# Performance work log

Measured on AMD Instinct MI355X. Metric: run time of the kernel, lower is better.

Reference implementation:

```python
import jax, jax.numpy as jnp
import numpy as np
import math

NUM_HEADS = 16
HEAD_SIZE = 64
QKT_MEAN = 0.0
QKT_STD = 0.05
APPLY_NOISE = True
NOISE_KEY = jax.random.key(42)


def quantize_activation_8bit(x):
    max_abs = jnp.maximum(jnp.max(jnp.abs(x)), 1e-08)
    scale = max_abs / 127.0
    return jnp.clip(jnp.round(x / scale), -127, 127) * scale


def quantize_weight_4bit(w):
    max_abs = jnp.maximum(jnp.max(jnp.abs(w)), 1e-08)
    scale = max_abs / 7.0
    return jnp.clip(jnp.round(w / scale), -7, 7) * scale


def setup_inputs() -> dict:
    key = jax.random.key(0)
    k1, k2, k3, k4 = jax.random.split(key, 4)
    B, S, D = 4, 1024, 1024
    hidden_states = jax.random.normal(k1, (B, S, D), dtype=jnp.float32)
    attention_mask = jnp.zeros((B, 1, 1, S), dtype=jnp.float32)
    # nn.Linear weights are [out_features, in_features]
    w_scale = 1.0 / math.sqrt(D)
    Wq = jax.random.normal(k2, (D, D), dtype=jnp.float32) * w_scale
    Wk = jax.random.normal(k3, (D, D), dtype=jnp.float32) * w_scale
    Wv = jax.random.normal(k4, (D, D), dtype=jnp.float32) * w_scale
    return {"hidden_states": hidden_states, "attention_mask": attention_mask,
            "Wq": Wq, "Wk": Wk, "Wv": Wv}


def _split_heads(x):
    B, S, _ = x.shape
    return x.reshape(B, S, NUM_HEADS, HEAD_SIZE).transpose(0, 2, 1, 3)  # [B,H,S,Dh]


def reference(hidden_states, attention_mask, Wq, Wk, Wv):
    h_q = quantize_activation_8bit(hidden_states)
    h_k = quantize_activation_8bit(hidden_states)
    Q = _split_heads(jnp.einsum('bsd,od->bso', h_q, quantize_weight_4bit(Wq)))
    K = _split_heads(jnp.einsum('bsd,od->bso', h_k, quantize_weight_4bit(Wk)))
    V = _split_heads(jnp.einsum('bsd,od->bso', hidden_states, quantize_weight_4bit(Wv)))
    qkt = jnp.einsum('bhqd,bhkd->bhqk', Q, K) / math.sqrt(HEAD_SIZE)
    if APPLY_NOISE and QKT_STD > 0:
        noise = jax.random.normal(NOISE_KEY, qkt.shape, dtype=qkt.dtype) * QKT_STD + QKT_MEAN
        qkt = qkt + noise
    qkt = qkt + attention_mask  # [B,1,1,S] broadcasts over [B,H,S,S]
    attn_weights = jax.nn.softmax(qkt, axis=-1)  # dropout is identity in eval
    ctx = jnp.einsum('bhqk,bhkd->bhqd', attn_weights, V)
    B, H, S, Dh = ctx.shape
    ctx = ctx.transpose(0, 2, 1, 3).reshape(B, S, H * Dh)
    return ctx
```

## Files before the change

### kernel.cpp

```cpp
#include <hip/hip_runtime.h>
#include <hip/hip_bf16.h>

typedef unsigned short u16;
typedef unsigned int u32;
typedef __bf16 bf16x8 __attribute__((ext_vector_type(8)));
typedef float f32x4 __attribute__((ext_vector_type(4)));

#define MFMA16(a, b, c) __builtin_amdgcn_mfma_f32_16x16x32_bf16((a), (b), (c), 0, 0, 0)

static __device__ __forceinline__ float bfbits2f(u32 b) {
    union { u32 u; float f; } c; c.u = b << 16; return c.f;
}
static __device__ __forceinline__ u32 f2bfbits(float f) {
    union { float f; u32 u; } c; c.f = f;
    return (c.u + 0x7FFFu + ((c.u >> 16) & 1u)) >> 16;
}
static __device__ __forceinline__ u32 f2bfbits_exact(float f) {
    union { float f; u32 u; } c; c.f = f;
    return c.u >> 16;
}
static __device__ __forceinline__ u32 pack_bf16x2(float lo, float hi) {
    float2 v; v.x = lo; v.y = hi;
    union { __hip_bfloat162 h; u32 u; } c;
    c.h = __float22bfloat162_rn(v);
    return c.u;
}

static __device__ __forceinline__ void noise_pu8(const u32* __restrict__ idx,
                                                 float* __restrict__ pu) {
    const u32 K1 = 42u, K2 = 0x1BD11BF0u;
    u32 x0[8], x1[8];
#pragma unroll
    for (int d = 0; d < 8; d++) { x0[d] = 0u; x1[d] = idx[d] + K1; }
#define TFR(R)                                            \
    _Pragma("unroll") for (int d = 0; d < 8; d++) {       \
        x0[d] += x1[d];                                   \
        x1[d] = __builtin_rotateleft32(x1[d], R) ^ x0[d]; \
    }
#define INJ(A, B)                                         \
    _Pragma("unroll") for (int d = 0; d < 8; d++) {       \
        x0[d] += (A); x1[d] += (B);                       \
    }
    TFR(13) TFR(15) TFR(26) TFR(6)  INJ(K1, K2 + 1u)
    TFR(17) TFR(29) TFR(16) TFR(24) INJ(K2, 2u)
    TFR(13) TFR(15) TFR(26) TFR(6)  INJ(0u, K1 + 3u)
    TFR(17) TFR(29) TFR(16) TFR(24) INJ(K1, K2 + 4u)
    TFR(13) TFR(15) TFR(26) TFR(6)  INJ(K2, 5u)
#undef TFR
#undef INJ
#pragma unroll
    for (int d = 0; d < 8; d++) {
        u32 bits = x0[d] ^ x1[d];
        float v2 = __uint_as_float((bits >> 9) | 0x40000000u);
        float u = v2 - 3.0f;
        float t = fmaf(-u, u, 1.0f);
        float L2 = __log2f(t);
        L2 = fmaxf(L2, -7.2134752f);
        float z = fmaf(L2, -0.69314718f, -2.5f);
        float p = 2.81022636e-08f;
        p = fmaf(p, z, 3.43273939e-07f);
        p = fmaf(p, z, -3.5233877e-06f);
        p = fmaf(p, z, -4.39150654e-06f);
        p = fmaf(p, z, 0.00021858087f);
        p = fmaf(p, z, -0.00125372503f);
        p = fmaf(p, z, -0.00417768164f);
        p = fmaf(p, z, 0.246640727f);
        p = fmaf(p, z, 1.50140941f);
        pu[d] = p * u;
    }
}

__global__ __launch_bounds__(256) void absmax_k(const float* __restrict__ h,
                                                const float* __restrict__ wq,
                                                const float* __restrict__ wk,
                                                const float* __restrict__ wv,
                                                u32* __restrict__ slots) {
    int t = blockIdx.y;
    const float* src = (t == 0) ? h : (t == 1) ? wq : (t == 2) ? wk : wv;
    int n4 = ((t == 0) ? 4096 * 1024 : 1024 * 1024) / 4;
    u32 mx = 0;
    int tid = threadIdx.x;
    for (int i = blockIdx.x * blockDim.x + tid; i < n4; i += gridDim.x * blockDim.x) {
        uint4 v = ((const uint4*)src)[i];
        mx = max(mx, v.x & 0x7FFFFFFFu);
        mx = max(mx, v.y & 0x7FFFFFFFu);
        mx = max(mx, v.z & 0x7FFFFFFFu);
        mx = max(mx, v.w & 0x7FFFFFFFu);
    }
    __shared__ u32 red[256];
    red[tid] = mx;
    __syncthreads();
    for (int s = 128; s > 0; s >>= 1) {
        if (tid < s) red[tid] = max(red[tid], red[tid + s]);
        __syncthreads();
    }
    if (tid == 0) atomicMax(&slots[t], red[0]);
}

__global__ __launch_bounds__(256) void prequant_all(const float* __restrict__ hidden,
                                                    const float* __restrict__ wq,
                                                    const float* __restrict__ wk,
                                                    const float* __restrict__ wv,
                                                    u16* __restrict__ hq,
                                                    u16* __restrict__ hbf,
                                                    u16* __restrict__ wqi,
                                                    u16* __restrict__ wki,
                                                    u16* __restrict__ wvi,
                                                    const u32* __restrict__ slots) {
    int y = blockIdx.y;
    const float* src = (y == 0) ? hidden : (y == 1) ? wq : (y == 2) ? wk : wv;
    u16* dqi = (y == 0) ? hq : (y == 1) ? wqi : (y == 2) ? wki : wvi;
    u16* draw = (y == 0) ? hbf : nullptr;
    float qmax = (y == 0) ? 127.0f : 7.0f;
    int n8 = ((y == 0) ? 4096 * 1024 : 1024 * 1024) / 8;

    float amax = fmaxf(__uint_as_float(slots[y]), 1e-8f);
    float scale = amax / qmax;
    for (int i = blockIdx.x * blockDim.x + threadIdx.x; i < n8; i += gridDim.x * blockDim.x) {
        float4 a = ((const float4*)src)[2 * i];
        float4 b = ((const float4*)src)[2 * i + 1];
        float x[8] = {a.x, a.y, a.z, a.w, b.x, b.y, b.z, b.w};
        u16 qi[8], rw[8];
#pragma unroll
        for (int j = 0; j < 8; j++) {
            float q = fminf(fmaxf(rintf(x[j] / scale), -qmax), qmax);
            qi[j] = (u16)f2bfbits_exact(q);
            rw[j] = (u16)f2bfbits(x[j]);
        }
        *(uint4*)(dqi + 8 * (size_t)i) = *(const uint4*)qi;
        if (draw) *(uint4*)(draw + 8 * (size_t)i) = *(const uint4*)rw;
    }
}

__global__ __launch_bounds__(256, 2) void qkv_gemm_all(const u16* __restrict__ hq,
                                                       const u16* __restrict__ hbf,
                                                       const u16* __restrict__ wqi,
                                                       const u16* __restrict__ wki,
                                                       const u16* __restrict__ wvi,
                                                       const u32* __restrict__ slots,
                                                       u16* __restrict__ Qb,
                                                       u16* __restrict__ Kb,
                                                       u16* __restrict__ Vtb) {
    __shared__ __align__(16) u16 As[128 * 40];
    __shared__ __align__(16) u16 Bs[128 * 40];
    int z = blockIdx.z;
    const u16* A  = (z < 2) ? hq : hbf;
    const u16* Bw = (z == 0) ? wqi : (z == 1) ? wki : wvi;
    u16* outp     = (z == 0) ? Qb : (z == 1) ? Kb : Vtb;
    int transOut = (z == 2);
    float s_a = fmaxf(__uint_as_float(slots[0]), 1e-8f) / 127.0f;
    float s_w = fmaxf(__uint_as_float(slots[z + 1]), 1e-8f) / 7.0f;
    float oscale = (z < 2) ? (s_a * s_w) : s_w;

    int tid = threadIdx.x;
    int srow = tid >> 2, scol = (tid & 3) * 8;
    int mbase = blockIdx.x * 128, nbase = blockIdx.y * 128;
    int lane = tid & 63, w = tid >> 6;
    int wv_m = w & 1, wv_n = w >> 1;
    int quad = lane >> 4, l16 = lane & 15;

    f32x4 acc[4][4];
#pragma unroll
    for (int i = 0; i < 4; i++)
#pragma unroll
        for (int j = 0; j < 4; j++) acc[i][j] = (f32x4){0.f, 0.f, 0.f, 0.f};

    const u16* aptr0 = A + (size_t)(mbase + srow) * 1024 + scol;
    const u16* aptr1 = A + (size_t)(mbase + 64 + srow) * 1024 + scol;
    const u16* bptr0 = Bw + (size_t)(nbase + srow) * 1024 + scol;
    const u16* bptr1 = Bw + (size_t)(nbase + 64 + srow) * 1024 + scol;

    for (int k0 = 0; k0 < 1024; k0 += 32) {
        uint4 a0 = *(const uint4*)(aptr0 + k0);
        uint4 a1 = *(const uint4*)(aptr1 + k0);
        uint4 b0 = *(const uint4*)(bptr0 + k0);
        uint4 b1 = *(const uint4*)(bptr1 + k0);
        __syncthreads();
        *(uint4*)(As + srow * 40 + scol) = a0;
        *(uint4*)(As + (64 + srow) * 40 + scol) = a1;
        *(uint4*)(Bs + srow * 40 + scol) = b0;
        *(uint4*)(Bs + (64 + srow) * 40 + scol) = b1;
        __syncthreads();
        bf16x8 af[4], bfr[4];
#pragma unroll
        for (int mt = 0; mt < 4; mt++)
            af[mt] = *(const bf16x8*)(As + (wv_m * 64 + mt * 16 + l16) * 40 + quad * 8);
#pragma unroll
        for (int nt = 0; nt < 4; nt++)
            bfr[nt] = *(const bf16x8*)(Bs + (wv_n * 64 + nt * 16 + l16) * 40 + quad * 8);
#pragma unroll
        for (int mt = 0; mt < 4; mt++)
#pragma unroll
            for (int nt = 0; nt < 4; nt++)
                acc[mt][nt] = MFMA16(af[mt], bfr[nt], acc[mt][nt]);
    }

#pragma unroll
    for (int mt = 0; mt < 4; mt++)
#pragma unroll
        for (int nt = 0; nt < 4; nt++)
#pragma unroll
            for (int r = 0; r < 4; r++) {
                float val = acc[mt][nt][r] * oscale;
                int m = mbase + wv_m * 64 + mt * 16 + quad * 4 + r;
                int o = nbase + wv_n * 64 + nt * 16 + l16;
                int b = m >> 10, s = m & 1023;
                int hh = o >> 6, dh = o & 63;
                size_t off = transOut ? (((size_t)(b * 16 + hh) * 64 + dh) * 1024 + s)
                                      : (((size_t)(b * 16 + hh) * 1024 + s) * 64 + dh);
                outp[off] = (u16)f2bfbits(val);
            }
}

__global__ __launch_bounds__(256, 2) void attn_kernel(const u16* __restrict__ Q,
                                                      const u16* __restrict__ K,
                                                      const u16* __restrict__ Vt,
                                                      const float* __restrict__ mask,
                                                      float* __restrict__ O0,
                                                      float* __restrict__ O1,
                                                      float* __restrict__ l0,
                                                      float* __restrict__ l1) {
    __shared__ __align__(16) u16 Plds[2][4][16][40];
    int qt = blockIdx.x, h = blockIdx.y;
    int b = blockIdx.z & 3, split = blockIdx.z >> 2;
    int bh = b * 16 + h;
    int tid = threadIdx.x, wv = tid >> 6, lane = tid & 63;
    int quad = lane >> 4, l16 = lane & 15;
    int q0 = qt * 64 + wv * 16;
    int ks0 = split * 512;

    float* Obuf = split ? O1 : O0;
    float* lbuf = split ? l1 : l0;

    const u16* Qb = Q + (size_t)bh * 1024 * 64;
    const u16* Kb = K + (size_t)bh * 1024 * 64;
    const u16* Vb = Vt + (size_t)bh * 64 * 1024;

    bf16x8 aq0 = *(const bf16x8*)(Qb + (q0 + l16) * 64 + quad * 8);
    bf16x8 aq1 = *(const bf16x8*)(Qb + (q0 + l16) * 64 + 32 + quad * 8);

    f32x4 oacc[4];
#pragma unroll
    for (int i = 0; i < 4; i++) oacc[i] = (f32x4){0.f, 0.f, 0.f, 0.f};
    float lsum[4] = {0.f, 0.f, 0.f, 0.f};

    u16* Pw0 = &Plds[0][wv][0][0];
    u16* Pw1 = &Plds[1][wv][0][0];
    u32 idxbase = ((u32)bh * 1024u + (u32)(q0 + quad * 4)) * 1024u;
    const float* maskb = mask + b * 1024;

    for (int ks = ks0; ks < ks0 + 512; ks += 32) {
        f32x4 s0 = (f32x4){0.f, 0.f, 0.f, 0.f};
        f32x4 s1 = (f32x4){0.f, 0.f, 0.f, 0.f};
        const u16* Kt = Kb + (size_t)ks * 64;
        bf16x8 bk0 = *(const bf16x8*)(Kt + l16 * 64 + quad * 8);
        bf16x8 bk1 = *(const bf16x8*)(Kt + l16 * 64 + 32 + quad * 8);
        bf16x8 bk2 = *(const bf16x8*)(Kt + (16 + l16) * 64 + quad * 8);
        bf16x8 bk3 = *(const bf16x8*)(Kt + (16 + l16) * 64 + 32 + quad * 8);
        s0 = MFMA16(aq0, bk0, s0);
        s0 = MFMA16(aq1, bk1, s0);
        s1 = MFMA16(aq0, bk2, s1);
        s1 = MFMA16(aq1, bk3, s1);

        int kg0 = ks + l16;
        float mk0 = maskb[kg0];
        float mk1 = maskb[kg0 + 16];

        u32 idxs[8];
        float pu[8];
#pragma unroll
        for (int r = 0; r < 4; r++) {
            u32 idx = idxbase + (u32)r * 1024u + (u32)kg0;
            idxs[2 * r] = idx;
            idxs[2 * r + 1] = idx + 16u;
        }
        noise_pu8(idxs, pu);

        u16* myP = ((ks >> 5) & 1) ? Pw1 : Pw0;
#pragma unroll
        for (int r = 0; r < 4; r++) {
            float sv0 = fmaf(pu[2 * r], 0.07071067811865475f, fmaf(s0[r], 0.125f, mk0));
            float sv1 = fmaf(pu[2 * r + 1], 0.07071067811865475f, fmaf(s1[r], 0.125f, mk1));
            float e0 = __expf(sv0);
            float e1 = __expf(sv1);
            u32 pk = pack_bf16x2(e0, e1);
            myP[(quad * 4 + r) * 40 + l16] = (u16)pk;
            myP[(quad * 4 + r) * 40 + 16 + l16] = (u16)(pk >> 16);
            lsum[r] += e0 + e1;
        }

        asm volatile("" ::: "memory");
        bf16x8 pf = *(const bf16x8*)(myP + l16 * 40 + quad * 8);
        asm volatile("" ::: "memory");
        const u16* Vk = Vb + ks;
#pragma unroll
        for (int nt = 0; nt < 4; nt++) {
            bf16x8 vf = *(const bf16x8*)(Vk + (nt * 16 + l16) * 1024 + quad * 8);
            oacc[nt] = MFMA16(pf, vf, oacc[nt]);
        }
    }

    float lred[4];
#pragma unroll
    for (int r = 0; r < 4; r++) {
        float l = lsum[r];
        l += __shfl_xor(l, 1);
        l += __shfl_xor(l, 2);
        l += __shfl_xor(l, 4);
        l += __shfl_xor(l, 8);
        lred[r] = l;
    }
    if (l16 == 0) {
        int lbase = bh * 1024 + q0 + quad * 4;
#pragma unroll
        for (int r = 0; r < 4; r++) lbuf[lbase + r] = lred[r];
    }
#pragma unroll
    for (int nt = 0; nt < 4; nt++) {
#pragma unroll
        for (int r = 0; r < 4; r++) {
            int q = q0 + quad * 4 + r;
            int dh = nt * 16 + l16;
            Obuf[((size_t)(b * 1024 + q)) * 1024 + h * 64 + dh] = oacc[nt][r];
        }
    }
}

__global__ __launch_bounds__(256) void combine_k(float* __restrict__ outp,
                                                 const float* __restrict__ O1,
                                                 const float* __restrict__ l0,
                                                 const float* __restrict__ l1) {
    int gid = blockIdx.x * 256 + threadIdx.x;
    int e = gid << 2;
    int bq = e >> 10;
    int h = (e & 1023) >> 6;
    int b = bq >> 10, q = bq & 1023;
    int lidx = ((b * 16 + h) << 10) + q;
    float linv = 1.0f / (l0[lidx] + l1[lidx]);
    float4 a = ((const float4*)outp)[gid];
    float4 c = ((const float4*)O1)[gid];
    float4 o;
    o.x = (a.x + c.x) * linv;
    o.y = (a.y + c.y) * linv;
    o.z = (a.z + c.z) * linv;
    o.w = (a.w + c.w) * linv;
    ((float4*)outp)[gid] = o;
}

extern "C" void kernel_launch(void* const* d_in, const int* in_sizes, int n_in,
                              void* d_out, int out_size, void* d_ws, size_t ws_size,
                              hipStream_t stream) {
    (void)in_sizes; (void)n_in; (void)out_size; (void)ws_size;
    const float* hidden = (const float*)d_in[0];
    const float* maskp  = (const float*)d_in[1];
    const float* Wq     = (const float*)d_in[2];
    const float* Wk     = (const float*)d_in[3];
    const float* Wv     = (const float*)d_in[4];
    float* outp = (float*)d_out;

    char* ws = (char*)d_ws;
    u32* slots = (u32*)ws;
    u16* hq  = (u16*)(ws + 256);
    u16* hbf = hq + 4096 * 1024;
    u16* wqi = hbf + 4096 * 1024;
    u16* wki = wqi + 1024 * 1024;
    u16* wvi = wki + 1024 * 1024;
    u16* Qb  = wvi + 1024 * 1024;
    u16* Kb  = Qb + 4096 * 1024;
    u16* Vtb = Kb + 4096 * 1024;

    float* O1buf = (float*)hq;
    float* l0buf = (float*)wqi;
    float* l1buf = l0buf + 4 * 16 * 1024;

    hipMemsetAsync(slots, 0, 16, stream);
    absmax_k<<<dim3(128, 4), 256, 0, stream>>>(hidden, Wq, Wk, Wv, slots);
    prequant_all<<<dim3(64, 4), 256, 0, stream>>>(hidden, Wq, Wk, Wv,
                                                  hq, hbf, wqi, wki, wvi, slots);
    qkv_gemm_all<<<dim3(32, 8, 3), 256, 0, stream>>>(hq, hbf, wqi, wki, wvi, slots,
                                                     Qb, Kb, Vtb);
    attn_kernel<<<dim3(16, 16, 8), 256, 0, stream>>>(Qb, Kb, Vtb, maskp,
                                                     outp, O1buf, l0buf, l1buf);
    combine_k<<<dim3(4096), 256, 0, stream>>>(outp, O1buf, l0buf, l1buf);
}
```

Baseline: 348.5 us.

## Transpose QK^T MFMA to keep P in registers and streamline Threefry noise

Swaps MFMA operand order so each lane holds scores for one query row across eight keys, which lets P feed the PV MFMA straight from registers instead of going through LDS. It also simplifies Threefry by folding the zero-key first round and merging key injection into the next round, uses alignbit rotates, and switches to base-2 exponent with prescaled constants and a mask prescaled into LDS. V loads are hoisted before the score math and occupancy is raised to 4 blocks. The main risks are register pressure at the higher occupancy and exact equivalence of the reordered Threefry and key-permuted V layout.

```diff
diff --git a/kernel.cpp b/kernel.cpp
--- a/kernel.cpp
+++ b/kernel.cpp
@@ -4,13 +4,11 @@
 typedef unsigned short u16;
 typedef unsigned int u32;
 typedef __bf16 bf16x8 __attribute__((ext_vector_type(8)));
+typedef __bf16 bf16x4 __attribute__((ext_vector_type(4)));
 typedef float f32x4 __attribute__((ext_vector_type(4)));
 
 #define MFMA16(a, b, c) __builtin_amdgcn_mfma_f32_16x16x32_bf16((a), (b), (c), 0, 0, 0)
 
-static __device__ __forceinline__ float bfbits2f(u32 b) {
-    union { u32 u; float f; } c; c.u = b << 16; return c.f;
-}
 static __device__ __forceinline__ u32 f2bfbits(float f) {
     union { float f; u32 u; } c; c.f = f;
     return (c.u + 0x7FFFu + ((c.u >> 16) & 1u)) >> 16;
@@ -26,31 +24,46 @@
     return c.u;
 }
 
-static __device__ __forceinline__ void noise_pu8(const u32* __restrict__ idx,
-                                                 float* __restrict__ pu) {
+static __device__ __forceinline__ u32 rotl_ab(u32 x, int r) {
+    return __builtin_amdgcn_alignbit(x, x, 32 - r);
+}
+
+static __device__ __forceinline__ float exp2_fast(float x) {
+    float r;
+    asm("v_exp_f32 %0, %1\n\ts_nop 1" : "=v"(r) : "v"(x));
+    return r;
+}
+
+static __device__ __forceinline__ void noise_pu8(u32 tk, float* __restrict__ pu) {
     const u32 K1 = 42u, K2 = 0x1BD11BF0u;
     u32 x0[8], x1[8];
 #pragma unroll
-    for (int d = 0; d < 8; d++) { x0[d] = 0u; x1[d] = idx[d] + K1; }
-#define TFR(R)                                            \
-    _Pragma("unroll") for (int d = 0; d < 8; d++) {       \
-        x0[d] += x1[d];                                   \
-        x1[d] = __builtin_rotateleft32(x1[d], R) ^ x0[d]; \
-    }
-#define INJ(A, B)                                         \
-    _Pragma("unroll") for (int d = 0; d < 8; d++) {       \
-        x0[d] += (A); x1[d] += (B);                       \
-    }
-    TFR(13) TFR(15) TFR(26) TFR(6)  INJ(K1, K2 + 1u)
-    TFR(17) TFR(29) TFR(16) TFR(24) INJ(K2, 2u)
-    TFR(13) TFR(15) TFR(26) TFR(6)  INJ(0u, K1 + 3u)
-    TFR(17) TFR(29) TFR(16) TFR(24) INJ(K1, K2 + 4u)
-    TFR(13) TFR(15) TFR(26) TFR(6)  INJ(K2, 5u)
+    for (int d = 0; d < 8; d++) {
+        u32 a = tk + (u32)(d < 4 ? d : 12 + d);
+        x0[d] = a;
+        x1[d] = rotl_ab(a, 13) ^ a;
+    }
+#define TFR(R)                                             \
+    _Pragma("unroll") for (int d = 0; d < 8; d++) {        \
+        x0[d] += x1[d];                                    \
+        x1[d] = rotl_ab(x1[d], R) ^ x0[d];                 \
+    }
+#define TFRI(R, A, B)                                      \
+    _Pragma("unroll") for (int d = 0; d < 8; d++) {        \
+        x1[d] += (B);                                      \
+        x0[d] += (A) + x1[d];              \
+        x1[d] = rotl_ab(x1[d], R) ^ x0[d];                 \
+    }
+    TFR(15) TFR(26) TFR(6)
+    TFRI(17, K1, K2 + 1u) TFR(29) TFR(16) TFR(24)
+    TFRI(13, K2, 2u)      TFR(15) TFR(26) TFR(6)
+    TFRI(17, 0u, K1 + 3u) TFR(29) TFR(16) TFR(24)
+    TFRI(13, K1, K2 + 4u) TFR(15) TFR(26) TFR(6)
 #undef TFR
-#undef INJ
+#undef TFRI
 #pragma unroll
     for (int d = 0; d < 8; d++) {
-        u32 bits = x0[d] ^ x1[d];
+        u32 bits = (x0[d] + K2) ^ (x1[d] + 5u);
         float v2 = __uint_as_float((bits >> 9) | 0x40000000u);
         float u = v2 - 3.0f;
         float t = fmaf(-u, u, 1.0f);
@@ -212,7 +225,7 @@
             }
 }
 
-__global__ __launch_bounds__(256, 2) void attn_kernel(const u16* __restrict__ Q,
+__global__ __launch_bounds__(256, 4) void attn_kernel(const u16* __restrict__ Q,
                                                       const u16* __restrict__ K,
                                                       const u16* __restrict__ Vt,
                                                       const float* __restrict__ mask,
@@ -220,7 +233,7 @@
                                                       float* __restrict__ O1,
                                                       float* __restrict__ l0,
                                                       float* __restrict__ l1) {
-    __shared__ __align__(16) u16 Plds[2][4][16][40];
+    __shared__ float msk[512];
     int qt = blockIdx.x, h = blockIdx.y;
     int b = blockIdx.z & 3, split = blockIdx.z >> 2;
     int bh = b * 16 + h;
@@ -229,12 +242,17 @@
     int q0 = qt * 64 + wv * 16;
     int ks0 = split * 512;
 
+    const float IL2 = 1.4426950408889634f;
+    const float* maskb = mask + b * 1024 + ks0;
+    msk[tid] = maskb[tid] * IL2;
+    msk[tid + 256] = maskb[tid + 256] * IL2;
+    __syncthreads();
+
     float* Obuf = split ? O1 : O0;
     float* lbuf = split ? l1 : l0;
-
     const u16* Qb = Q + (size_t)bh * 1024 * 64;
     const u16* Kb = K + (size_t)bh * 1024 * 64;
-    const u16* Vb = Vt + (size_t)bh * 64 * 1024;
+    const u16* Vb = Vt + (size_t)bh * 64 * 1024 + ks0;
 
     bf16x8 aq0 = *(const bf16x8*)(Qb + (q0 + l16) * 64 + quad * 8);
     bf16x8 aq1 = *(const bf16x8*)(Qb + (q0 + l16) * 64 + 32 + quad * 8);
@@ -242,79 +260,68 @@
     f32x4 oacc[4];
 #pragma unroll
     for (int i = 0; i < 4; i++) oacc[i] = (f32x4){0.f, 0.f, 0.f, 0.f};
-    float lsum[4] = {0.f, 0.f, 0.f, 0.f};
-
-    u16* Pw0 = &Plds[0][wv][0][0];
-    u16* Pw1 = &Plds[1][wv][0][0];
-    u32 idxbase = ((u32)bh * 1024u + (u32)(q0 + quad * 4)) * 1024u;
-    const float* maskb = mask + b * 1024;
-
-    for (int ks = ks0; ks < ks0 + 512; ks += 32) {
-        f32x4 s0 = (f32x4){0.f, 0.f, 0.f, 0.f};
-        f32x4 s1 = (f32x4){0.f, 0.f, 0.f, 0.f};
-        const u16* Kt = Kb + (size_t)ks * 64;
+    float lsum = 0.f;
+
+    u32 tbase = ((u32)(bh * 1024 + q0 + l16)) * 1024u + (u32)ks0 + (u32)(4 * quad) + 42u;
+
+    const float C_S = 0.18033688011112042f;
+    const float C_N = 0.10201394645f;
+
+    for (int kk = 0; kk < 512; kk += 32) {
+        const u16* Kt = Kb + (size_t)(ks0 + kk) * 64;
         bf16x8 bk0 = *(const bf16x8*)(Kt + l16 * 64 + quad * 8);
         bf16x8 bk1 = *(const bf16x8*)(Kt + l16 * 64 + 32 + quad * 8);
         bf16x8 bk2 = *(const bf16x8*)(Kt + (16 + l16) * 64 + quad * 8);
         bf16x8 bk3 = *(const bf16x8*)(Kt + (16 + l16) * 64 + 32 + quad * 8);
-        s0 = MFMA16(aq0, bk0, s0);
-        s0 = MFMA16(aq1, bk1, s0);
-        s1 = MFMA16(aq0, bk2, s1);
-        s1 = MFMA16(aq1, bk3, s1);
-
-        int kg0 = ks + l16;
-        float mk0 = maskb[kg0];
-        float mk1 = maskb[kg0 + 16];
-
-        u32 idxs[8];
+
+        const u16* Vk = Vb + kk + 4 * quad;
+        bf16x4 vlo[4], vhi[4];
+#pragma unroll
+        for (int nt = 0; nt < 4; nt++) {
+            vlo[nt] = *(const bf16x4*)(Vk + (nt * 16 + l16) * 1024);
+            vhi[nt] = *(const bf16x4*)(Vk + (nt * 16 + l16) * 1024 + 16);
+        }
+
+        int mb = kk + 4 * quad;
+        float mk[4], mh[4];
+#pragma unroll
+        for (int r = 0; r < 4; r++) { mk[r] = msk[mb + r]; mh[r] = msk[mb + 16 + r]; }
+
         float pu[8];
+        noise_pu8(tbase + (u32)kk, pu);
+
+        f32x4 s0 = (f32x4){0.f, 0.f, 0.f, 0.f};
+        f32x4 s1 = (f32x4){0.f, 0.f, 0.f, 0.f};
+        s0 = MFMA16(bk0, aq0, s0);
+        s0 = MFMA16(bk1, aq1, s0);
+        s1 = MFMA16(bk2, aq0, s1);
+        s1 = MFMA16(bk3, aq1, s1);
+
+        float e[8];
 #pragma unroll
         for (int r = 0; r < 4; r++) {
-            u32 idx = idxbase + (u32)r * 1024u + (u32)kg0;
-            idxs[2 * r] = idx;
-            idxs[2 * r + 1] = idx + 16u;
-        }
-        noise_pu8(idxs, pu);
-
-        u16* myP = ((ks >> 5) & 1) ? Pw1 : Pw0;
-#pragma unroll
-        for (int r = 0; r < 4; r++) {
-            float sv0 = fmaf(pu[2 * r], 0.07071067811865475f, fmaf(s0[r], 0.125f, mk0));
-            float sv1 = fmaf(pu[2 * r + 1], 0.07071067811865475f, fmaf(s1[r], 0.125f, mk1));
-            float e0 = __expf(sv0);
-            float e1 = __expf(sv1);
-            u32 pk = pack_bf16x2(e0, e1);
-            myP[(quad * 4 + r) * 40 + l16] = (u16)pk;
-            myP[(quad * 4 + r) * 40 + 16 + l16] = (u16)(pk >> 16);
-            lsum[r] += e0 + e1;
-        }
-
-        asm volatile("" ::: "memory");
-        bf16x8 pf = *(const bf16x8*)(myP + l16 * 40 + quad * 8);
-        asm volatile("" ::: "memory");
-        const u16* Vk = Vb + ks;
+            e[r]     = exp2_fast(fmaf(pu[r],     C_N, fmaf(s0[r], C_S, mk[r])));
+            e[4 + r] = exp2_fast(fmaf(pu[4 + r], C_N, fmaf(s1[r], C_S, mh[r])));
+        }
+        lsum += ((e[0] + e[1]) + (e[2] + e[3])) + ((e[4] + e[5]) + (e[6] + e[7]));
+
+        union { u32 u[4]; bf16x8 v; } pf;
+        pf.u[0] = pack_bf16x2(e[0], e[1]);
+        pf.u[1] = pack_bf16x2(e[2], e[3]);
+        pf.u[2] = pack_bf16x2(e[4], e[5]);
+        pf.u[3] = pack_bf16x2(e[6], e[7]);
+
 #pragma unroll
         for (int nt = 0; nt < 4; nt++) {
-            bf16x8 vf = *(const bf16x8*)(Vk + (nt * 16 + l16) * 1024 + quad * 8);
-            oacc[nt] = MFMA16(pf, vf, oacc[nt]);
-        }
-    }
-
-    float lred[4];
-#pragma unroll
-    for (int r = 0; r < 4; r++) {
-        float l = lsum[r];
-        l += __shfl_xor(l, 1);
-        l += __shfl_xor(l, 2);
-        l += __shfl_xor(l, 4);
-        l += __shfl_xor(l, 8);
-        lred[r] = l;
-    }
-    if (l16 == 0) {
-        int lbase = bh * 1024 + q0 + quad * 4;
-#pragma unroll
-        for (int r = 0; r < 4; r++) lbuf[lbase + r] = lred[r];
-    }
+            bf16x8 vf = __builtin_shufflevector(vlo[nt], vhi[nt], 0, 1, 2, 3, 4, 5, 6, 7);
+            oacc[nt] = MFMA16(pf.v, vf, oacc[nt]);
+        }
+    }
+
+    float l = lsum;
+    l += __shfl_xor(l, 16);
+    l += __shfl_xor(l, 32);
+    if (lane < 16) lbuf[bh * 1024 + q0 + lane] = l;
 #pragma unroll
     for (int nt = 0; nt < 4; nt++) {
 #pragma unroll
```

Result: no change. 343.2 us (-1.5%).
